# Performance work log

Measured on AMD Instinct MI355X. Metric: run time of the kernel, lower is better.

The kernel has to match this reference:

```python
import jax, jax.numpy as jnp
import numpy as np

D = 1024
H = 16
B = 8
N = 1024


def setup_inputs() -> dict:
    key = jax.random.key(0)
    k1, k2, k3 = jax.random.split(key, 3)
    x = jax.random.normal(k1, (B, N, D), dtype=jnp.float32)
    w_in = jax.random.normal(k2, (D, 3 * D), dtype=jnp.float32) * (1.0 / np.sqrt(D))
    w_out = jax.random.normal(k3, (D, D), dtype=jnp.float32) * (1.0 / np.sqrt(D))
    b_out = jnp.zeros((D,), dtype=jnp.float32)
    return {"x": x, "w_in": w_in, "w_out": w_out, "b_out": b_out}


def reference(x, w_in, w_out, b_out):
    h = H
    d = D // H
    scale = D ** (-0.5)  # note: full dimension, per source
    qkv = x @ w_in  # [B, N, 3D]
    # rearrange 'b n (qkv h d) -> qkv b h n d'
    qkv = qkv.reshape(x.shape[0], x.shape[1], 3, h, d)
    qkv = jnp.transpose(qkv, (2, 0, 3, 1, 4))
    q, k, v = qkv[0], qkv[1], qkv[2]
    scores = jnp.einsum('bhid,bhjd->bhij', q, k) * scale
    attn = jax.nn.softmax(scores, axis=-1)
    out = jnp.einsum('bhij,bhjd->bhid', attn, v)
    # 'b h n d -> b n (h d)'
    out = jnp.transpose(out, (0, 2, 1, 3)).reshape(x.shape[0], x.shape[1], h * d)
    return out @ w_out + b_out
```

## Files before the change

### kernel.cpp

```cpp
#include <hip/hip_runtime.h>
#include <stdint.h>
#include <stddef.h>

typedef __bf16 bf16;
typedef __bf16 bf16x4 __attribute__((ext_vector_type(4)));
typedef __bf16 bf16x8 __attribute__((ext_vector_type(8)));
typedef float  f32x4  __attribute__((ext_vector_type(4)));
typedef float  f32x16 __attribute__((ext_vector_type(16)));
typedef float  f32x4v __attribute__((ext_vector_type(4)));

__device__ __forceinline__ void gload_lds16(const void* g, void* lds) {
  __builtin_amdgcn_global_load_lds(
      (__attribute__((address_space(1))) void*)(uintptr_t)g,
      (__attribute__((address_space(3))) void*)lds,
      16, 0, 0);
}


__global__ void cvt_f32_to_bf16(const float* __restrict__ in, bf16* __restrict__ out, int n) {
  int i = (blockIdx.x * blockDim.x + threadIdx.x) * 4;
  if (i >= n) return;
  f32x4v v = *reinterpret_cast<const f32x4v*>(in + i);
  bf16x4 o;
  o[0] = (bf16)v[0]; o[1] = (bf16)v[1]; o[2] = (bf16)v[2]; o[3] = (bf16)v[3];
  *reinterpret_cast<bf16x4*>(out + i) = o;
}

__global__ void transpose_cvt(const float* __restrict__ in, bf16* __restrict__ out, int R, int C) {
  __shared__ bf16 tile[32][33];
  int c0 = blockIdx.x * 32, r0 = blockIdx.y * 32;
  int tx = threadIdx.x, ty = threadIdx.y;
  #pragma unroll
  for (int i = ty; i < 32; i += 8)
    tile[i][tx] = (bf16)in[(size_t)(r0 + i) * C + (c0 + tx)];
  __syncthreads();
  #pragma unroll
  for (int i = ty; i < 32; i += 8)
    out[(size_t)(c0 + i) * R + (r0 + tx)] = tile[tx][i];
}


template <typename OT, bool BIAS>
__global__ __launch_bounds__(256) void gemm_abt(
    const bf16* __restrict__ A,
    const bf16* __restrict__ Bt,
    const float* __restrict__ bias,
    OT* __restrict__ C, int M, int N, int K)
{
  __shared__ bf16 As[128 * 64];
  __shared__ bf16 Bs[128 * 64];

  const int tid = threadIdx.x;
  const int w = tid >> 6, l = tid & 63;
  const int l15 = l & 15, l4 = l >> 4, l7 = l & 7;
  const int wr = w >> 1, wc = w & 1;

  const int nwgx = N >> 7;
  const int nwg  = (M >> 7) * nwgx;
  const int cpx  = nwg >> 3;
  const int bid  = blockIdx.x;
  const int swz  = (bid & 7) * cpx + (bid >> 3);
  const int m0 = (swz / nwgx) * 128, n0 = (swz % nwgx) * 128;

  f32x4 acc[4][4];
  #pragma unroll
  for (int i = 0; i < 4; i++)
    #pragma unroll
    for (int j = 0; j < 4; j++) acc[i][j] = (f32x4){0.f, 0.f, 0.f, 0.f};

  const int srow  = w * 8 + (l >> 3);
  const int sslot = (l & 7) ^ ((l >> 3) & 7);
  const int KT = K >> 6;

  for (int kt = 0; kt < KT; ++kt) {
    __syncthreads();
    const int kcol = kt * 64 + sslot * 8;
    #pragma unroll
    for (int p = 0; p < 4; ++p) {
      gload_lds16(A  + (size_t)(m0 + p * 32 + srow) * K + kcol,
                  (char*)As + p * 4096 + w * 1024);
      gload_lds16(Bt + (size_t)(n0 + p * 32 + srow) * K + kcol,
                  (char*)Bs + p * 4096 + w * 1024);
    }
    __syncthreads();

    #pragma unroll
    for (int kk = 0; kk < 2; ++kk) {
      const int coff = (kk * 32 + l4 * 8) ^ (l7 << 3);
      bf16x8 af[4], bq[4];
      #pragma unroll
      for (int m = 0; m < 4; ++m) {
        int r = wr * 64 + m * 16 + l15;
        af[m] = *reinterpret_cast<const bf16x8*>(&As[r * 64 + coff]);
      }
      #pragma unroll
      for (int n = 0; n < 4; ++n) {
        int r = wc * 64 + n * 16 + l15;
        bq[n] = *reinterpret_cast<const bf16x8*>(&Bs[r * 64 + coff]);
      }
      #pragma unroll
      for (int m = 0; m < 4; ++m)
        #pragma unroll
        for (int n = 0; n < 4; ++n)
          acc[m][n] = __builtin_amdgcn_mfma_f32_16x16x32_bf16(af[m], bq[n], acc[m][n], 0, 0, 0);
    }
  }

  #pragma unroll
  for (int m = 0; m < 4; ++m) {
    #pragma unroll
    for (int n = 0; n < 4; ++n) {
      int col = n0 + wc * 64 + n * 16 + l15;
      float bv = BIAS ? bias[col] : 0.f;
      #pragma unroll
      for (int j = 0; j < 4; ++j) {
        int row = m0 + wr * 64 + m * 16 + l4 * 4 + j;
        float v = acc[m][n][j] + bv;
        C[(size_t)row * N + col] = (OT)v;
      }
    }
  }
}


__global__ __launch_bounds__(512) void attn_fused(
    const bf16* __restrict__ qkv,
    bf16* __restrict__ aout)
{
  __shared__ bf16 Ks[64 * 64];
  __shared__ bf16 Vt[64 * 64];
  __shared__ bf16 Pl[8][32 * 64];

  const int tid = threadIdx.x;
  const int w = tid >> 6, l = tid & 63;
  const int l31 = l & 31, hi = l >> 5;

  const int bid = blockIdx.x;
  const int c  = bid & 7, rr = bid >> 3;
  const int g  = c * 16 + (rr & 15);
  const int qt = rr >> 4;
  const int h  = g & 15;
  const int b  = g >> 4;

  const bf16* base = qkv + (size_t)b * 1024 * 3072;
  const int qrow0 = qt * 256 + w * 32;

  const float qscale = 0.03125f * 1.44269504f;
  bf16x8 qf[4];
  #pragma unroll
  for (int st = 0; st < 4; st++) {
    const bf16* p = base + (size_t)(qrow0 + l31) * 3072 + h * 64 + st * 16 + hi * 8;
    bf16x8 v = *reinterpret_cast<const bf16x8*>(p);
    #pragma unroll
    for (int e = 0; e < 8; e++) v[e] = (bf16)((float)v[e] * qscale);
    qf[st] = v;
  }

  bf16x8 onesf;
  #pragma unroll
  for (int e = 0; e < 8; e++) onesf[e] = (bf16)1.0f;

  f32x16 acc0 = {}, acc1 = {}, accS = {};

  const int skey  = w * 8 + (l >> 3);
  const int sslot = (l & 7) ^ ((l >> 3) & 7);
  const int vd0   = (tid & 15) * 4;
  const int vk0   = ((tid >> 4) & 15) * 4;
  const int vslot = (tid >> 5) & 7;
  const int vhalf = (tid >> 4) & 1;

  for (int kt = 0; kt < 16; ++kt) {
    __syncthreads();
    gload_lds16(base + (size_t)(kt * 64 + skey) * 3072 + 1024 + h * 64 + sslot * 8,
                (char*)Ks + w * 1024);
    if (tid < 256) {
      bf16x4 vv[4];
      #pragma unroll
      for (int i = 0; i < 4; ++i)
        vv[i] = *reinterpret_cast<const bf16x4*>(
            base + (size_t)(kt * 64 + vk0 + i) * 3072 + 2048 + h * 64 + vd0);
      #pragma unroll
      for (int j = 0; j < 4; ++j) {
        int d = vd0 + j;
        bf16x4 o; o[0] = vv[0][j]; o[1] = vv[1][j]; o[2] = vv[2][j]; o[3] = vv[3][j];
        *reinterpret_cast<bf16x4*>(
            &Vt[d * 64 + ((vslot ^ (d & 7) ^ ((d >> 3) & 7)) * 8 + vhalf * 4)]) = o;
      }
    }
    __syncthreads();

    #pragma unroll
    for (int ktile = 0; ktile < 2; ++ktile) {
      f32x16 s = {};
      const int key = ktile * 32 + l31;
      #pragma unroll
      for (int st = 0; st < 4; ++st) {
        const int slot = (2 * st + hi) ^ (key & 7);
        bf16x8 kf = *reinterpret_cast<const bf16x8*>(&Ks[key * 64 + slot * 8]);
        s = __builtin_amdgcn_mfma_f32_32x32x16_bf16(kf, qf[st], s, 0, 0, 0);
      }
      #pragma unroll
      for (int gq = 0; gq < 4; ++gq) {
        bf16x4 pb;
        #pragma unroll
        for (int j2 = 0; j2 < 4; ++j2) {
          float pv = __builtin_amdgcn_exp2f(s[4 * gq + j2]);
          pb[j2] = (bf16)pv;
        }
        const int chunk = ktile * 4 + gq;
        *reinterpret_cast<bf16x4*>(
            &Pl[w][l31 * 64 + ((chunk ^ (l31 & 7)) * 8 + hi * 4)]) = pb;
      }
    }

    const int d7x0 = (l31 & 7) ^ (l31 >> 3);
    const int d7x1 = d7x0 ^ 4;
    #pragma unroll
    for (int st = 0; st < 4; ++st) {
      const int cs = 2 * st + hi;
      bf16x8 pa  = *reinterpret_cast<const bf16x8*>(
          &Pl[w][l31 * 64 + ((cs ^ (l31 & 7)) * 8)]);
      accS = __builtin_amdgcn_mfma_f32_32x32x16_bf16(pa, onesf, accS, 0, 0, 0);
      bf16x8 vf0 = *reinterpret_cast<const bf16x8*>(
          &Vt[l31 * 64 + ((cs ^ d7x0) * 8)]);
      acc0 = __builtin_amdgcn_mfma_f32_32x32x16_bf16(pa, vf0, acc0, 0, 0, 0);
      bf16x8 vf1 = *reinterpret_cast<const bf16x8*>(
          &Vt[(32 + l31) * 64 + ((cs ^ d7x1) * 8)]);
      acc1 = __builtin_amdgcn_mfma_f32_32x32x16_bf16(pa, vf1, acc1, 0, 0, 0);
    }
  }

  #pragma unroll
  for (int reg = 0; reg < 16; ++reg) {
    int q_r = (reg & 3) + 8 * (reg >> 2) + 4 * hi;
    float rinv = 1.0f / accS[reg];
    size_t rowoff = ((size_t)b * 1024 + qrow0 + q_r) * 1024 + h * 64;
    aout[rowoff + l31]      = (bf16)(acc0[reg] * rinv);
    aout[rowoff + 32 + l31] = (bf16)(acc1[reg] * rinv);
  }
}


extern "C" void kernel_launch(void* const* d_in, const int* in_sizes, int n_in,
                              void* d_out, int out_size, void* d_ws, size_t ws_size,
                              hipStream_t stream) {
  const float* x     = (const float*)d_in[0];
  const float* w_in  = (const float*)d_in[1];
  const float* w_out = (const float*)d_in[2];
  const float* b_out = (const float*)d_in[3];
  float* out = (float*)d_out;

  bf16* xb    = (bf16*)d_ws;
  bf16* wint  = xb    + (size_t)8192 * 1024;
  bf16* woutt = wint  + (size_t)3072 * 1024;
  bf16* qkv   = woutt + (size_t)1024 * 1024;
  bf16* ao    = qkv   + (size_t)8192 * 3072;

  cvt_f32_to_bf16<<<8192, 256, 0, stream>>>(x, xb, 8192 * 1024);
  transpose_cvt<<<dim3(96, 32), dim3(32, 8), 0, stream>>>(w_in,  wint,  1024, 3072);
  transpose_cvt<<<dim3(32, 32), dim3(32, 8), 0, stream>>>(w_out, woutt, 1024, 1024);

  gemm_abt<bf16, false><<<1536, 256, 0, stream>>>(xb, wint, nullptr, qkv, 8192, 3072, 1024);

  attn_fused<<<512, 512, 0, stream>>>(qkv, ao);

  gemm_abt<float, true><<<512, 256, 0, stream>>>(ao, woutt, b_out, out, 8192, 1024, 1024);
}
```

Baseline: 159.8 us.

## Use 256x256 double-buffered pipelined GEMM for QKV projection

Adds a new GEMM kernel with 256x256 tiles, 512 threads and double-buffered LDS. It splits each k-step into four quadrant phases and issues next-tile global-to-LDS loads between them, using manual waitcnt/barrier and setprio around the MFMA blocks. The goal is more reuse per tile and hiding load latency behind MFMA work in the QKV projection. In exchange it raises LDS use to 128KB and register pressure, and launches only 384 workgroups at one per CU, so occupancy and tail balance could suffer.

```diff
diff --git a/kernel.cpp b/kernel.cpp
--- a/kernel.cpp
+++ b/kernel.cpp
@@ -120,6 +120,138 @@
       }
     }
   }
+}
+
+
+template <typename OT, bool BIAS>
+__global__ __launch_bounds__(512, 1) void gemm256(
+    const bf16* __restrict__ A,
+    const bf16* __restrict__ Bt,
+    const float* __restrict__ bias,
+    OT* __restrict__ C, int M, int N, int K)
+{
+  __shared__ bf16 As[2][256 * 64];
+  __shared__ bf16 Bs[2][256 * 64];
+
+  const int tid = threadIdx.x;
+  const int w = tid >> 6, l = tid & 63;
+  const int l15 = l & 15, l4 = l >> 4, l7 = l & 7;
+  const int wm = w >> 2, wn = w & 3;
+
+  const int nwgx = N >> 8;
+  const int nwg  = (M >> 8) * nwgx;
+  const int cpx  = nwg >> 3;
+  const int bid  = blockIdx.x;
+  const int swz  = (bid & 7) * cpx + (bid >> 3);
+  const int m0 = (swz / nwgx) * 256, n0 = (swz % nwgx) * 256;
+
+  f32x4 acc[8][4];
+  #pragma unroll
+  for (int i = 0; i < 8; i++)
+    #pragma unroll
+    for (int j = 0; j < 4; j++) acc[i][j] = (f32x4){0.f, 0.f, 0.f, 0.f};
+
+  const int w8l   = w * 8 + (l >> 3);
+  const int sslot = (l & 7) ^ ((l >> 3) & 7);
+  const int KT = K >> 6;
+
+  #define STA(t, hoff)                                                          \
+    _Pragma("unroll")                                                           \
+    for (int q = 0; q < 2; ++q)                                                 \
+      gload_lds16(A + (size_t)(m0 + (hoff) + q * 64 + w8l) * K + (t) * 64 + sslot * 8, \
+                  (char*)As[(t) & 1] + (hoff) * 128 + q * 8192 + w * 1024);
+  #define STB(t, hoff)                                                          \
+    _Pragma("unroll")                                                           \
+    for (int q = 0; q < 2; ++q)                                                 \
+      gload_lds16(Bt + (size_t)(n0 + (hoff) + q * 64 + w8l) * K + (t) * 64 + sslot * 8, \
+                  (char*)Bs[(t) & 1] + (hoff) * 128 + q * 8192 + w * 1024);
+
+  STA(0, 0); STB(0, 0); STB(0, 128); STA(0, 128);
+
+  bf16x8 afr[4][2], bfr[2][2];
+
+  #define PHASE(buf, mh, nh)                                                     \
+    {                                                                            \
+      __builtin_amdgcn_s_setprio(1);                                             \
+      if ((nh) == 0) {                                                           \
+        _Pragma("unroll")                                                        \
+        for (int i = 0; i < 4; ++i)                                              \
+          _Pragma("unroll")                                                      \
+          for (int kk = 0; kk < 2; ++kk) {                                       \
+            int r = (mh) * 128 + wm * 64 + i * 16 + l15;                         \
+            afr[i][kk] = *reinterpret_cast<const bf16x8*>(                       \
+                &As[buf][r * 64 + (((kk * 4 + l4) ^ l7) * 8)]);                  \
+          }                                                                      \
+      }                                                                          \
+      _Pragma("unroll")                                                          \
+      for (int n2 = 0; n2 < 2; ++n2)                                             \
+        _Pragma("unroll")                                                        \
+        for (int kk = 0; kk < 2; ++kk) {                                         \
+          int r = (nh) * 128 + wn * 32 + n2 * 16 + l15;                          \
+          bfr[n2][kk] = *reinterpret_cast<const bf16x8*>(                        \
+              &Bs[buf][r * 64 + (((kk * 4 + l4) ^ l7) * 8)]);                    \
+        }                                                                        \
+      _Pragma("unroll")                                                          \
+      for (int i = 0; i < 4; ++i)                                                \
+        _Pragma("unroll")                                                        \
+        for (int n2 = 0; n2 < 2; ++n2)                                           \
+          _Pragma("unroll")                                                      \
+          for (int kk = 0; kk < 2; ++kk)                                         \
+            acc[(mh) * 4 + i][(nh) * 2 + n2] =                                   \
+                __builtin_amdgcn_mfma_f32_16x16x32_bf16(                         \
+                    afr[i][kk], bfr[n2][kk], acc[(mh) * 4 + i][(nh) * 2 + n2],   \
+                    0, 0, 0);                                                    \
+      __builtin_amdgcn_s_setprio(0);                                             \
+    }
+
+  for (int t = 0; t < KT - 1; ++t) {
+    const int buf = t & 1;
+    STA(t + 1, 0);
+    asm volatile("s_waitcnt vmcnt(6)" ::: "memory");
+    asm volatile("s_barrier" ::: "memory");
+    PHASE(buf, 0, 0)
+    STB(t + 1, 0);
+    asm volatile("s_waitcnt vmcnt(6)" ::: "memory");
+    asm volatile("s_barrier" ::: "memory");
+    PHASE(buf, 0, 1)
+    STB(t + 1, 128);
+    asm volatile("s_waitcnt vmcnt(6)" ::: "memory");
+    asm volatile("s_barrier" ::: "memory");
+    PHASE(buf, 1, 0)
+    STA(t + 1, 128);
+    asm volatile("s_barrier" ::: "memory");
+    PHASE(buf, 1, 1)
+  }
+
+  asm volatile("s_waitcnt vmcnt(0)" ::: "memory");
+  asm volatile("s_barrier" ::: "memory");
+  {
+    const int buf = (KT - 1) & 1;
+    PHASE(buf, 0, 0)
+    PHASE(buf, 0, 1)
+    PHASE(buf, 1, 0)
+    PHASE(buf, 1, 1)
+  }
+  #undef PHASE
+  #undef STA
+  #undef STB
+
+  #pragma unroll
+  for (int mh = 0; mh < 2; ++mh)
+    #pragma unroll
+    for (int i = 0; i < 4; ++i)
+      #pragma unroll
+      for (int nh = 0; nh < 2; ++nh)
+        #pragma unroll
+        for (int n2 = 0; n2 < 2; ++n2) {
+          int col = n0 + nh * 128 + wn * 32 + n2 * 16 + l15;
+          float bv = BIAS ? bias[col] : 0.f;
+          #pragma unroll
+          for (int j = 0; j < 4; ++j) {
+            int row = m0 + mh * 128 + wm * 64 + i * 16 + l4 * 4 + j;
+            C[(size_t)row * N + col] = (OT)(acc[mh * 4 + i][nh * 2 + n2][j] + bv);
+          }
+        }
 }
 
 
@@ -260,7 +392,7 @@
   transpose_cvt<<<dim3(96, 32), dim3(32, 8), 0, stream>>>(w_in,  wint,  1024, 3072);
   transpose_cvt<<<dim3(32, 32), dim3(32, 8), 0, stream>>>(w_out, woutt, 1024, 1024);
 
-  gemm_abt<bf16, false><<<1536, 256, 0, stream>>>(xb, wint, nullptr, qkv, 8192, 3072, 1024);
+  gemm256<bf16, false><<<384, 512, 0, stream>>>(xb, wint, nullptr, qkv, 8192, 3072, 1024);
 
   attn_fused<<<512, 512, 0, stream>>>(qkv, ao);
 
```

Result: no change. 162.3 us (median of 2 runs) (+1.6%).
